# Performance work log

Hardware: AMD Instinct MI355X
Metric: run time of the kernel (lower is better)

The kernel has to match this reference:

```python
import jax, jax.numpy as jnp
import numpy as np
from functools import reduce

IN_CH = 1; OUT_CH = 16; K = 3; PAD = 1; QDEPTH = 2; WIRES = 4; DIM = 2 ** WIRES

# --- precomputed CNOT permutation matrices (constants) ---
# PennyLane convention: wire 0 is the most significant bit of the basis index.
def _cnot_mat(control, target):
    perm = np.arange(DIM)
    cbit = 1 << (WIRES - 1 - control)
    tbit = 1 << (WIRES - 1 - target)
    flip = (perm & cbit).astype(bool)
    perm = np.where(flip, perm ^ tbit, perm)
    return jnp.asarray(np.eye(DIM, dtype=np.complex64)[perm])

# StronglyEntanglingLayers default ranges: r_l = l % (n_wires - 1) + 1
_CNOTS = [[_cnot_mat(i, (i + (l % (WIRES - 1) + 1)) % WIRES) for i in range(WIRES)]
          for l in range(QDEPTH)]

def _rot(angles):
    # qml.Rot(phi, theta, omega) = RZ(omega) @ RY(theta) @ RZ(phi)
    phi, theta, omega = angles[0], angles[1], angles[2]
    c = jnp.cos(theta / 2); s = jnp.sin(theta / 2)
    return jnp.stack([
        jnp.exp(-0.5j * (phi + omega)) * c, -jnp.exp(0.5j * (phi - omega)) * s,
        jnp.exp(-0.5j * (phi - omega)) * s,  jnp.exp(0.5j * (phi + omega)) * c,
    ]).reshape(2, 2)

def _sel_unitary(weights):
    # Full 16x16 unitary of StronglyEntanglingLayers(weights) -- dim is tiny,
    # so building the dense unitary once and batching patches through it is
    # the efficient form (vs. per-gate contractions over 2.1M state vectors).
    U = jnp.eye(DIM, dtype=jnp.complex64)
    for l in range(QDEPTH):
        layer = reduce(jnp.kron, [_rot(weights[l, i]) for i in range(WIRES)])
        U = layer @ U
        for C in _CNOTS[l]:
            U = C @ U
    return U

def setup_inputs() -> dict:
    key = jax.random.key(0)
    k1, k2 = jax.random.split(key)
    x = jax.random.normal(k1, (32, 1, 256, 256), dtype=jnp.float32)
    weights = jax.random.uniform(k2, (QDEPTH, WIRES, 3), dtype=jnp.float32)
    return {"x": x, "weights": weights}

def reference(x, weights):
    b, c, h_in, w_in = x.shape
    h_out = h_in + 2 * PAD - K + 1
    w_out = w_in + 2 * PAD - K + 1
    # ConstantPad2d with value 0.01
    xp = jnp.pad(x, ((0, 0), (0, 0), (PAD, PAD), (PAD, PAD)), constant_values=0.01)
    # unfold -> (b, c*K*K, h_out, w_out), feature order (c, k0, k1)
    patches = jax.lax.conv_general_dilated_patches(xp, (K, K), (1, 1), 'VALID')
    patches = patches.transpose(0, 2, 3, 1).reshape(b * h_out * w_out, K * K)
    # zero-pad patch vectors from K*K=9 to 2^wires=16, then L2-normalize (eps=1e-12)
    patches = jnp.pad(patches, ((0, 0), (0, DIM - K * K)))
    norm = jnp.linalg.norm(patches, axis=-1, keepdims=True)
    patches = patches / jnp.maximum(norm, 1e-12)
    # Mottonen prep on |0> yields the normalized patch exactly (up to global
    # phase); then apply the entangling-layer unitary and measure probs.
    state = patches.astype(jnp.complex64) @ _sel_unitary(weights).T  # (N, 16)
    probs = jnp.abs(state) ** 2
    out = jnp.clip(probs * (DIM * 0.5), 0.0, 1.0)[:, :OUT_CH]
    return out.reshape(b, h_out, w_out, OUT_CH).transpose(0, 3, 1, 2)
```

## Files before the change

### kernel.cpp

```cpp
#include <hip/hip_runtime.h>
#include <math.h>


#define WIRES 4
#define DIM 16

__device__ inline void rot_entry(float phi, float th, float om, int rb, int cb,
                                 float& er, float& ei) {
    float a = 0.5f * (phi + om);
    float b = 0.5f * (phi - om);
    float ss, cc;
    sincosf(0.5f * th, &ss, &cc);
    float ang = (rb ^ cb) ? b : a;
    float sa, ca;
    sincosf(ang, &sa, &ca);
    float mag = (rb ^ cb) ? ss : cc;
    er = ((rb == 0) && (cb == 1)) ? (-mag * ca) : (mag * ca);
    ei = ((rb & cb) ? mag : -mag) * sa;
}

__device__ inline void layer_elem(const float* __restrict__ w, int l, int r,
                                  int c, float& pr, float& pi) {
    pr = 1.f; pi = 0.f;
    #pragma unroll
    for (int i = 0; i < WIRES; ++i) {
        const float* wi = w + (l * WIRES + i) * 3;
        float er, ei;
        int rb = (r >> (3 - i)) & 1, cb = (c >> (3 - i)) & 1;
        rot_entry(wi[0], wi[1], wi[2], rb, cb, er, ei);
        float nr = pr * er - pi * ei;
        float ni = pr * ei + pi * er;
        pr = nr; pi = ni;
    }
}

__device__ inline int cnot_src(int r, int range) {
    int src = r;
    #pragma unroll
    for (int i = WIRES - 1; i >= 0; --i) {
        int control = i, target = (i + range) & 3;
        int cbit = 1 << (3 - control), tbit = 1 << (3 - target);
        if (src & cbit) src ^= tbit;
    }
    return src;
}

#define H 256
#define W 256
#define NB 32
#define OUTC 16
#define RPB 4

__global__ __launch_bounds__(256) void qconv_kernel(
        const float* __restrict__ x, const float* __restrict__ w,
        float* __restrict__ out) {
    __shared__ float L0r[DIM][DIM], L0i[DIM][DIM];
    __shared__ float L1r[DIM][DIM], L1i[DIM][DIM];
    __shared__ float sU[OUTC][20];
    __shared__ float rows[RPB + 2][W + 8];

    int t = threadIdx.x;
    int blk = blockIdx.x;
    int b = blk >> 6;
    int i0 = (blk & 63) << 2;

    const float* xb = x + (size_t)b * (H * W);
    #pragma unroll
    for (int wr = 0; wr < RPB + 2; ++wr) {
        int row = i0 + wr - 1;
        bool rok = (unsigned)row < (unsigned)H;
        for (int cpos = t; cpos < W + 2; cpos += 256) {
            int j = cpos - 1;
            float v = 0.01f;
            if (rok && (unsigned)j < (unsigned)W) v = xb[row * W + j];
            rows[wr][cpos] = v;
        }
    }

    int ur = t >> 4, uc = t & 15;
    {
        float lr, li;
        layer_elem(w, 0, ur, uc, lr, li);
        L0r[ur][uc] = lr; L0i[ur][uc] = li;
        layer_elem(w, 1, ur, uc, lr, li);
        L1r[ur][uc] = lr; L1i[ur][uc] = li;
    }
    __syncthreads();
    if (uc < 9) {
        int s1 = cnot_src(ur, 2);
        float ar = 0.f, ai = 0.f;
        #pragma unroll
        for (int m = 0; m < DIM; ++m) {
            int p0 = cnot_src(m, 1);
            float xr = L1r[s1][m], xi = L1i[s1][m];
            float yr = L0r[p0][uc], yi = L0i[p0][uc];
            ar += xr * yr - xi * yi;
            ai += xr * yi + xi * yr;
        }
        sU[ur][2 * uc]     = ar;
        sU[ur][2 * uc + 1] = ai;
    }
    __syncthreads();

    int rl = t >> 6;
    int c  = (t & 63) << 2;
    int i  = i0 + rl;

    float win[3][6];
    #pragma unroll
    for (int di = 0; di < 3; ++di) {
        float4 a = *(const float4*)&rows[rl + di][c];
        float4 bq = *(const float4*)&rows[rl + di][c + 4];
        win[di][0] = a.x;  win[di][1] = a.y;  win[di][2] = a.z;
        win[di][3] = a.w;  win[di][4] = bq.x; win[di][5] = bq.y;
    }

    float fac[4];
    #pragma unroll
    for (int px = 0; px < 4; ++px) {
        float n2 = 0.f;
        #pragma unroll
        for (int di = 0; di < 3; ++di)
            #pragma unroll
            for (int dj = 0; dj < 3; ++dj) {
                float pv = win[di][px + dj];
                n2 = fmaf(pv, pv, n2);
            }
        fac[px] = 8.0f / fmaxf(n2, 1e-24f);
    }

    float* ob = out + (size_t)b * OUTC * (H * W) + (size_t)i * W + c;
    #pragma unroll
    for (int k = 0; k < OUTC; ++k) {
        float4 q0 = *(const float4*)&sU[k][0];
        float4 q1 = *(const float4*)&sU[k][4];
        float4 q2 = *(const float4*)&sU[k][8];
        float4 q3 = *(const float4*)&sU[k][12];
        float2 q4 = *(const float2*)&sU[k][16];
        float4 res;
        #pragma unroll
        for (int px = 0; px < 4; ++px) {
            float sr, si;
            sr = q0.x * win[0][px];
            si = q0.y * win[0][px];
            sr = fmaf(q0.z, win[0][px + 1], sr);
            si = fmaf(q0.w, win[0][px + 1], si);
            sr = fmaf(q1.x, win[0][px + 2], sr);
            si = fmaf(q1.y, win[0][px + 2], si);
            sr = fmaf(q1.z, win[1][px], sr);
            si = fmaf(q1.w, win[1][px], si);
            sr = fmaf(q2.x, win[1][px + 1], sr);
            si = fmaf(q2.y, win[1][px + 1], si);
            sr = fmaf(q2.z, win[1][px + 2], sr);
            si = fmaf(q2.w, win[1][px + 2], si);
            sr = fmaf(q3.x, win[2][px], sr);
            si = fmaf(q3.y, win[2][px], si);
            sr = fmaf(q3.z, win[2][px + 1], sr);
            si = fmaf(q3.w, win[2][px + 1], si);
            sr = fmaf(q4.x, win[2][px + 2], sr);
            si = fmaf(q4.y, win[2][px + 2], si);
            float v = fac[px] * fmaf(sr, sr, si * si);
            ((float*)&res)[px] = fminf(v, 1.0f);
        }
        *(float4*)&ob[(size_t)k * (H * W)] = res;
    }
}

extern "C" void kernel_launch(void* const* d_in, const int* in_sizes, int n_in,
                              void* d_out, int out_size, void* d_ws, size_t ws_size,
                              hipStream_t stream) {
    const float* x = (const float*)d_in[0];
    const float* w = (const float*)d_in[1];
    float* out = (float*)d_out;

    qconv_kernel<<<NB * H / RPB, 256, 0, stream>>>(x, w, out);
}
```

Baseline: 145.9 us.

## Precompute rotation entries once and double rows per block

Each block used to compute every 16x16 layer-matrix entry with eight sincosf calls per entry. Now 32 threads compute the 2x2 rotation entries into shared memory and the kron products are assembled from them. Blocks also grow to 512 threads covering 8 output rows, which halves the number of blocks that redundantly rebuild the unitary. This adds an extra barrier and a larger halo tile, and only half the threads take part in building the unitary.

```diff
diff --git a/kernel.cpp b/kernel.cpp
--- a/kernel.cpp
+++ b/kernel.cpp
@@ -4,35 +4,6 @@
 
 #define WIRES 4
 #define DIM 16
-
-__device__ inline void rot_entry(float phi, float th, float om, int rb, int cb,
-                                 float& er, float& ei) {
-    float a = 0.5f * (phi + om);
-    float b = 0.5f * (phi - om);
-    float ss, cc;
-    sincosf(0.5f * th, &ss, &cc);
-    float ang = (rb ^ cb) ? b : a;
-    float sa, ca;
-    sincosf(ang, &sa, &ca);
-    float mag = (rb ^ cb) ? ss : cc;
-    er = ((rb == 0) && (cb == 1)) ? (-mag * ca) : (mag * ca);
-    ei = ((rb & cb) ? mag : -mag) * sa;
-}
-
-__device__ inline void layer_elem(const float* __restrict__ w, int l, int r,
-                                  int c, float& pr, float& pi) {
-    pr = 1.f; pi = 0.f;
-    #pragma unroll
-    for (int i = 0; i < WIRES; ++i) {
-        const float* wi = w + (l * WIRES + i) * 3;
-        float er, ei;
-        int rb = (r >> (3 - i)) & 1, cb = (c >> (3 - i)) & 1;
-        rot_entry(wi[0], wi[1], wi[2], rb, cb, er, ei);
-        float nr = pr * er - pi * ei;
-        float ni = pr * ei + pi * er;
-        pr = nr; pi = ni;
-    }
-}
 
 __device__ inline int cnot_src(int r, int range) {
     int src = r;
@@ -49,11 +20,13 @@
 #define W 256
 #define NB 32
 #define OUTC 16
-#define RPB 4
+#define RPB 8
+#define TPB 512
 
-__global__ __launch_bounds__(256) void qconv_kernel(
+__global__ __launch_bounds__(TPB) void qconv_kernel(
         const float* __restrict__ x, const float* __restrict__ w,
         float* __restrict__ out) {
+    __shared__ float2 sRot[2][WIRES][2][2];
     __shared__ float L0r[DIM][DIM], L0i[DIM][DIM];
     __shared__ float L1r[DIM][DIM], L1i[DIM][DIM];
     __shared__ float sU[OUTC][20];
@@ -61,15 +34,15 @@
 
     int t = threadIdx.x;
     int blk = blockIdx.x;
-    int b = blk >> 6;
-    int i0 = (blk & 63) << 2;
+    int b = blk >> 5;
+    int i0 = (blk & 31) << 3;
 
     const float* xb = x + (size_t)b * (H * W);
     #pragma unroll
     for (int wr = 0; wr < RPB + 2; ++wr) {
         int row = i0 + wr - 1;
         bool rok = (unsigned)row < (unsigned)H;
-        for (int cpos = t; cpos < W + 2; cpos += 256) {
+        for (int cpos = t; cpos < W + 2; cpos += TPB) {
             int j = cpos - 1;
             float v = 0.01f;
             if (rok && (unsigned)j < (unsigned)W) v = xb[row * W + j];
@@ -77,16 +50,43 @@
         }
     }
 
-    int ur = t >> 4, uc = t & 15;
-    {
-        float lr, li;
-        layer_elem(w, 0, ur, uc, lr, li);
-        L0r[ur][uc] = lr; L0i[ur][uc] = li;
-        layer_elem(w, 1, ur, uc, lr, li);
-        L1r[ur][uc] = lr; L1i[ur][uc] = li;
+    if (t < 32) {
+        int l = t >> 4, i = (t >> 2) & 3, rb = (t >> 1) & 1, cb = t & 1;
+        const float* wi = w + (l * WIRES + i) * 3;
+        float phi = wi[0], th = wi[1], om = wi[2];
+        float a = 0.5f * (phi + om);
+        float bb = 0.5f * (phi - om);
+        float ss, cc;
+        sincosf(0.5f * th, &ss, &cc);
+        float ang = (rb ^ cb) ? bb : a;
+        float sa, ca;
+        sincosf(ang, &sa, &ca);
+        float mag = (rb ^ cb) ? ss : cc;
+        float er = ((rb == 0) && (cb == 1)) ? (-mag * ca) : (mag * ca);
+        float ei = ((rb & cb) ? mag : -mag) * sa;
+        sRot[l][i][rb][cb] = make_float2(er, ei);
     }
     __syncthreads();
-    if (uc < 9) {
+
+    int ur = t >> 4, uc = t & 15;
+    if (t < 256) {
+        #pragma unroll
+        for (int l = 0; l < 2; ++l) {
+            float pr = 1.f, pi = 0.f;
+            #pragma unroll
+            for (int i = 0; i < WIRES; ++i) {
+                int rb = (ur >> (3 - i)) & 1, cb = (uc >> (3 - i)) & 1;
+                float2 e = sRot[l][i][rb][cb];
+                float nr = pr * e.x - pi * e.y;
+                float ni = pr * e.y + pi * e.x;
+                pr = nr; pi = ni;
+            }
+            if (l == 0) { L0r[ur][uc] = pr; L0i[ur][uc] = pi; }
+            else        { L1r[ur][uc] = pr; L1i[ur][uc] = pi; }
+        }
+    }
+    __syncthreads();
+    if (t < 256 && uc < 9) {
         int s1 = cnot_src(ur, 2);
         float ar = 0.f, ai = 0.f;
         #pragma unroll
@@ -173,5 +173,5 @@
     const float* w = (const float*)d_in[1];
     float* out = (float*)d_out;
 
-    qconv_kernel<<<NB * H / RPB, 256, 0, stream>>>(x, w, out);
+    qconv_kernel<<<NB * H / RPB, TPB, 0, stream>>>(x, w, out);
 }
```

New measurement: 145.7 us (median of 2 runs). No clear change (-0.2%).
